# Performance work log

Hardware: AMD Instinct MI355X
Metric: run time of the kernel (lower is better)

The kernel has to match this reference:

```python
import jax, jax.numpy as jnp
import numpy as np

DIM = 2048
NUM_HEADS = 16
HEAD_DIM = 128
MAX_SEQ_LEN = 2048
ATTN_SCALE = 0.12
EPS = 1e-6


def _rms_norm(x):
    # RMSNorm without learned weight, over last dim
    return x * jax.lax.rsqrt(jnp.mean(jnp.square(x), axis=-1, keepdims=True) + EPS)


def _rope_tables(T):
    # half of the head dim rotates, half is identity (zero frequency)
    quarter = HEAD_DIM // 4
    angular_freq = (1.0 / 1024.0) ** jnp.linspace(0.0, 1.0, quarter, dtype=jnp.float32)
    angular_freq = jnp.concatenate([angular_freq, jnp.zeros(quarter, dtype=jnp.float32)])  # [D/2]
    t = jnp.arange(T, dtype=jnp.float32)
    theta = t[:, None] * angular_freq[None, :]  # [T, D/2]
    return jnp.cos(theta), jnp.sin(theta)


def _apply_rope(x, cos, sin):
    # x: [B, T, H, D]; cos/sin: [T, D/2] -> broadcast [1, T, 1, D/2]
    x1, x2 = jnp.split(x, 2, axis=-1)
    c = cos[None, :, None, :]
    s = sin[None, :, None, :]
    y1 = x1 * c + x2 * s
    y2 = -x1 * s + x2 * c
    return jnp.concatenate([y1, y2], axis=-1)


def setup_inputs() -> dict:
    key = jax.random.key(0)
    k1, k2, k3, k4 = jax.random.split(key, 4)
    hdim = NUM_HEADS * HEAD_DIM
    x = jax.random.normal(k1, (1, MAX_SEQ_LEN, DIM), dtype=jnp.float32)
    qkvo_w = jax.random.normal(k2, (4, hdim, DIM), dtype=jnp.float32) * (DIM ** -0.5)
    ve = jax.random.normal(k3, (1, MAX_SEQ_LEN, hdim), dtype=jnp.float32)
    lambdas = jax.random.uniform(k4, (2,), dtype=jnp.float32)
    return {"x": x, "qkvo_w": qkvo_w, "ve": ve, "lambdas": lambdas}


def reference(x, qkvo_w, ve, lambdas):
    B, T, _ = x.shape
    H, D = NUM_HEADS, HEAD_DIM
    # fused qkv projection: [B, T, 3*H*D]
    qkv = jnp.einsum('btc,ehc->bteh', x, qkvo_w[:3]).reshape(B, T, 3, H, D)
    q, k, v = qkv[:, :, 0], qkv[:, :, 1], qkv[:, :, 2]  # each [B, T, H, D]
    q, k, v = _rms_norm(q), _rms_norm(k), _rms_norm(v)
    cos, sin = _rope_tables(T)
    q = _apply_rope(q, cos, sin)
    k = _apply_rope(k, cos, sin)
    v = lambdas[0] * v + lambdas[1] * ve.reshape(B, T, H, D)
    # causal attention with fixed scale
    scores = jnp.einsum('bthd,bshd->bhts', q, k) * ATTN_SCALE  # [B, H, T, T]
    causal = jnp.tril(jnp.ones((T, T), dtype=bool))
    scores = jnp.where(causal[None, None], scores, -jnp.inf)
    p = jax.nn.softmax(scores, axis=-1)
    y = jnp.einsum('bhts,bshd->bthd', p, v).reshape(B, T, H * D)
    return jnp.einsum('bth,ch->btc', y, qkvo_w[3])
```

## Files before the change

### kernel.cpp

```cpp
#include <hip/hip_runtime.h>
#include <math.h>

#define SEQ  2048
#define CDIM 2048
#define NH   16
#define DH   128
#define HDIM 2048

typedef __attribute__((ext_vector_type(8))) short  bf16x8;
typedef __attribute__((ext_vector_type(4))) float  f32x4;
typedef unsigned short ushort_t;

__device__ __forceinline__ unsigned short f2bf(float f) {
  unsigned u = __float_as_uint(f);
  u = (u + 0x7fffu + ((u >> 16) & 1u)) >> 16;
  return (unsigned short)u;
}
__device__ __forceinline__ float b2f(unsigned short s) {
  return __uint_as_float((unsigned)s << 16);
}

__device__ __forceinline__ void async_ld16(const ushort_t* g, ushort_t* l) {
  __builtin_amdgcn_global_load_lds((const __attribute__((address_space(1))) unsigned int*)g,
                                   (__attribute__((address_space(3))) unsigned int*)l,
                                   16, 0, 0);
}

__device__ __forceinline__ f32x4 mfma16(bf16x8 a, bf16x8 b, f32x4 c) {
  return __builtin_amdgcn_mfma_f32_16x16x32_bf16(a, b, c, 0, 0, 0);
}

__global__ __launch_bounds__(256) void to_bf16(const float* __restrict__ src,
                                               ushort_t* __restrict__ dst, int n8) {
  int i = blockIdx.x * 256 + threadIdx.x;
  if (i >= n8) return;
  const float4* s = (const float4*)src;
  float4 f0 = s[i * 2], f1 = s[i * 2 + 1];
  bf16x8 o;
  o[0] = (short)f2bf(f0.x); o[1] = (short)f2bf(f0.y);
  o[2] = (short)f2bf(f0.z); o[3] = (short)f2bf(f0.w);
  o[4] = (short)f2bf(f1.x); o[5] = (short)f2bf(f1.y);
  o[6] = (short)f2bf(f1.z); o[7] = (short)f2bf(f1.w);
  *(bf16x8*)&dst[i * 8] = o;
}

template <int OUT_BF16>
__global__ __launch_bounds__(256) void gemm_bf16(const ushort_t* __restrict__ A,
                                                 const ushort_t* __restrict__ B,
                                                 void* __restrict__ Cv,
                                                 long bStride, long cStride) {
  constexpr int K = CDIM, N = HDIM;
  __shared__ __align__(16) ushort_t As[128 * 32];
  __shared__ __align__(16) ushort_t Bs[128 * 32];
  const ushort_t* Bp = B + (long)blockIdx.z * bStride;
  const int m0 = blockIdx.y * 128, n0 = blockIdx.x * 128;
  const int tid = threadIdx.x, lane = tid & 63, wave = tid >> 6;
  const int wm = wave >> 1, wn = wave & 1;
  const int g = lane >> 4, l15 = lane & 15;
  const int srow = tid >> 2, scc = tid & 3;

  f32x4 acc[4][4];
#pragma unroll
  for (int i = 0; i < 4; ++i)
#pragma unroll
    for (int j = 0; j < 4; ++j) acc[i][j] = (f32x4)0.0f;

  for (int k0 = 0; k0 < K; k0 += 32) {
    __syncthreads();
    {
      int r0 = srow, r1 = srow + 64;
      int c0 = scc ^ ((r0 >> 1) & 3), c1 = scc ^ ((r1 >> 1) & 3);
      async_ld16(&A [(long)(m0 + r0) * K + k0 + c0 * 8], &As[wave * 512]);
      async_ld16(&A [(long)(m0 + r1) * K + k0 + c1 * 8], &As[2048 + wave * 512]);
      async_ld16(&Bp[(long)(n0 + r0) * K + k0 + c0 * 8], &Bs[wave * 512]);
      async_ld16(&Bp[(long)(n0 + r1) * K + k0 + c1 * 8], &Bs[2048 + wave * 512]);
    }
    __syncthreads();

    bf16x8 af[4], bfr[4];
#pragma unroll
    for (int mi = 0; mi < 4; ++mi) {
      int row = wm * 64 + mi * 16 + l15;
      int cc = g ^ ((row >> 1) & 3);
      af[mi] = *(const bf16x8*)&As[row * 32 + cc * 8];
    }
#pragma unroll
    for (int ni = 0; ni < 4; ++ni) {
      int row = wn * 64 + ni * 16 + l15;
      int cc = g ^ ((row >> 1) & 3);
      bfr[ni] = *(const bf16x8*)&Bs[row * 32 + cc * 8];
    }
#pragma unroll
    for (int mi = 0; mi < 4; ++mi)
#pragma unroll
      for (int ni = 0; ni < 4; ++ni)
        acc[mi][ni] = mfma16(af[mi], bfr[ni], acc[mi][ni]);
  }

#pragma unroll
  for (int mi = 0; mi < 4; ++mi)
#pragma unroll
    for (int ni = 0; ni < 4; ++ni) {
      int row = m0 + wm * 64 + mi * 16 + g * 4;
      int col = n0 + wn * 64 + ni * 16 + l15;
#pragma unroll
      for (int r = 0; r < 4; ++r) {
        if (OUT_BF16)
          ((ushort_t*)Cv)[cStride * blockIdx.z + (long)(row + r) * N + col] = f2bf(acc[mi][ni][r]);
        else
          ((float*)Cv)[(long)(row + r) * N + col] = acc[mi][ni][r];
      }
    }
}

__device__ __forceinline__ float wave_sum64(float x) {
#pragma unroll
  for (int m = 32; m >= 1; m >>= 1) x += __shfl_xor(x, m, 64);
  return x;
}

__global__ __launch_bounds__(64) void norm_rope(ushort_t* __restrict__ qkvb,
                                                const float* __restrict__ ve,
                                                const float* __restrict__ lambdas) {
  const int t = blockIdx.x, h = blockIdx.y, d = threadIdx.x;
  const long base = (long)t * HDIM + h * DH;
  ushort_t* q = qkvb + base;
  ushort_t* k = qkvb + (long)SEQ * HDIM + base;
  ushort_t* v = qkvb + 2L * SEQ * HDIM + base;

  float q1 = b2f(q[d]), q2 = b2f(q[d + 64]);
  float k1 = b2f(k[d]), k2 = b2f(k[d + 64]);
  float v1 = b2f(v[d]), v2 = b2f(v[d + 64]);

  float qsc = rsqrtf(wave_sum64(q1 * q1 + q2 * q2) * (1.0f / 128.0f) + 1e-6f);
  float ksc = rsqrtf(wave_sum64(k1 * k1 + k2 * k2) * (1.0f / 128.0f) + 1e-6f);
  float vsc = rsqrtf(wave_sum64(v1 * v1 + v2 * v2) * (1.0f / 128.0f) + 1e-6f);
  q1 *= qsc; q2 *= qsc;
  k1 *= ksc; k2 *= ksc;
  v1 *= vsc; v2 *= vsc;

  float freq = (d < 32) ? powf(1.0f / 1024.0f, (float)d * (1.0f / 31.0f)) : 0.0f;
  float th = (float)t * freq;
  float c = cosf(th), s = sinf(th);

  float qo1 = q1 * c + q2 * s, qo2 = -q1 * s + q2 * c;
  float ko1 = k1 * c + k2 * s, ko2 = -k1 * s + k2 * c;

  float l0 = lambdas[0], l1 = lambdas[1];
  const float* vep = ve + base;
  float vo1 = l0 * v1 + l1 * vep[d];
  float vo2 = l0 * v2 + l1 * vep[d + 64];

  q[d] = f2bf(qo1); q[d + 64] = f2bf(qo2);
  k[d] = f2bf(ko1); k[d + 64] = f2bf(ko2);
  v[d] = f2bf(vo1); v[d + 64] = f2bf(vo2);
}

__global__ __launch_bounds__(256) void transpose_v(const ushort_t* __restrict__ vb,
                                                   ushort_t* __restrict__ vbT) {
  __shared__ __align__(16) ushort_t L[64 * 136];
  const int t0 = blockIdx.x * 64, h = blockIdx.y;
  const int tid = threadIdx.x;
#pragma unroll
  for (int p = 0; p < 4; ++p) {
    int idx = p * 256 + tid;
    int row = idx >> 4, cc = idx & 15;
    *(bf16x8*)&L[row * 136 + cc * 8] =
        *(const bf16x8*)&vb[(long)(t0 + row) * HDIM + h * DH + cc * 8];
  }
  __syncthreads();
#pragma unroll
  for (int p = 0; p < 4; ++p) {
    int idx = p * 256 + tid;
    int d = idx >> 3, tc = (idx & 7) * 8;
    bf16x8 o;
#pragma unroll
    for (int j = 0; j < 8; ++j) o[j] = (short)L[(tc + j) * 136 + d];
    *(bf16x8*)&vbT[((long)h * DH + d) * SEQ + t0 + tc] = o;
  }
}

__global__ __launch_bounds__(128) void flash_mfma(const ushort_t* __restrict__ qkvb,
                                                  const ushort_t* __restrict__ vbT,
                                                  ushort_t* __restrict__ yb) {
  __shared__ __align__(16) ushort_t Ks[64 * 128];
  __shared__ __align__(16) ushort_t Vt[128 * 64];
  __shared__ __align__(16) ushort_t Ps[64 * 72];
  const int q0 = blockIdx.x * 64, h = blockIdx.y;
  const int tid = threadIdx.x, lane = tid & 63, wave = tid >> 6;
  const int g = lane >> 4, l15 = lane & 15;
  const ushort_t* Kg = qkvb + (long)SEQ * HDIM;
  const ushort_t* Vg = vbT + (long)h * DH * SEQ;

  bf16x8 qf[2][4];
#pragma unroll
  for (int nt = 0; nt < 2; ++nt)
#pragma unroll
    for (int ks = 0; ks < 4; ++ks)
      qf[nt][ks] = *(const bf16x8*)
          &qkvb[(long)(q0 + wave * 32 + nt * 16 + l15) * HDIM + h * DH + ks * 32 + g * 8];

  f32x4 oacc[2][8];
#pragma unroll
  for (int qt = 0; qt < 2; ++qt)
#pragma unroll
    for (int dt = 0; dt < 8; ++dt) oacc[qt][dt] = (f32x4)0.0f;
  float mrow[2] = {-1e30f, -1e30f}, lrow[2] = {0.0f, 0.0f};

  for (int s0 = 0; s0 <= q0; s0 += 64) {
    __syncthreads();
#pragma unroll
    for (int i = 0; i < 8; ++i) {
      int idx = i * 128 + tid;
      { int row = idx >> 4, cc = idx & 15, cg = cc ^ (row & 7);
        async_ld16(&Kg[(long)(s0 + row) * HDIM + h * DH + cg * 8], &Ks[i * 1024 + wave * 512]); }
      { int row = idx >> 3, cc = idx & 7,  cg = cc ^ (row & 7);
        async_ld16(&Vg[(long)row * SEQ + s0 + cg * 8], &Vt[i * 1024 + wave * 512]); }
    }
    __syncthreads();

    f32x4 st[2][4];
#pragma unroll
    for (int nt = 0; nt < 2; ++nt)
#pragma unroll
      for (int mt = 0; mt < 4; ++mt) st[nt][mt] = (f32x4)0.0f;
#pragma unroll
    for (int ks = 0; ks < 4; ++ks)
#pragma unroll
      for (int mt = 0; mt < 4; ++mt) {
        int row = mt * 16 + l15;
        int cg = ks * 4 + g;
        int cc = cg ^ (row & 7);
        bf16x8 a = *(const bf16x8*)&Ks[row * 128 + cc * 8];
        st[0][mt] = mfma16(a, qf[0][ks], st[0][mt]);
        st[1][mt] = mfma16(a, qf[1][ks], st[1][mt]);
      }

    float alpha_q[2];
#pragma unroll
    for (int nt = 0; nt < 2; ++nt) {
      const int qg = q0 + wave * 32 + nt * 16 + l15;
      float p[4][4];
      float tmax = -1e30f;
#pragma unroll
      for (int mt = 0; mt < 4; ++mt)
#pragma unroll
        for (int r = 0; r < 4; ++r) {
          float sv = st[nt][mt][r] * 0.12f;
          if (s0 + mt * 16 + g * 4 + r > qg) sv = -1e30f;
          p[mt][r] = sv;
          tmax = fmaxf(tmax, sv);
        }
      tmax = fmaxf(tmax, __shfl_xor(tmax, 16, 64));
      tmax = fmaxf(tmax, __shfl_xor(tmax, 32, 64));
      float nm = fmaxf(mrow[nt], tmax);
      float alpha = __expf(mrow[nt] - nm);
      float psum = 0.0f;
#pragma unroll
      for (int mt = 0; mt < 4; ++mt) {
        float e0 = __expf(p[mt][0] - nm), e1 = __expf(p[mt][1] - nm);
        float e2 = __expf(p[mt][2] - nm), e3 = __expf(p[mt][3] - nm);
        unsigned short b0 = f2bf(e0), b1 = f2bf(e1), b2 = f2bf(e2), b3 = f2bf(e3);
        psum += b2f(b0) + b2f(b1) + b2f(b2) + b2f(b3);
        unsigned lo = (unsigned)b0 | ((unsigned)b1 << 16);
        unsigned hi = (unsigned)b2 | ((unsigned)b3 << 16);
        *(uint2*)&Ps[(wave * 32 + nt * 16 + l15) * 72 + mt * 16 + g * 4] = make_uint2(lo, hi);
      }
      psum += __shfl_xor(psum, 16, 64);
      psum += __shfl_xor(psum, 32, 64);
      mrow[nt] = nm;
      lrow[nt] = lrow[nt] * alpha + psum;
      alpha_q[nt] = alpha;
    }

    float aO[2][4];
#pragma unroll
    for (int qt = 0; qt < 2; ++qt)
#pragma unroll
      for (int r = 0; r < 4; ++r)
        aO[qt][r] = __shfl(alpha_q[qt], g * 4 + r, 64);
#pragma unroll
    for (int qt = 0; qt < 2; ++qt)
#pragma unroll
      for (int dt = 0; dt < 8; ++dt)
#pragma unroll
        for (int r = 0; r < 4; ++r)
          oacc[qt][dt][r] *= aO[qt][r];

#pragma unroll
    for (int ks = 0; ks < 2; ++ks) {
      bf16x8 ap0 = *(const bf16x8*)&Ps[(wave * 32 + l15) * 72 + ks * 32 + g * 8];
      bf16x8 ap1 = *(const bf16x8*)&Ps[(wave * 32 + 16 + l15) * 72 + ks * 32 + g * 8];
#pragma unroll
      for (int dt = 0; dt < 8; ++dt) {
        int row = dt * 16 + l15;
        int cg = ks * 4 + g;
        int cc = cg ^ (row & 7);
        bf16x8 bv = *(const bf16x8*)&Vt[row * 64 + cc * 8];
        oacc[0][dt] = mfma16(ap0, bv, oacc[0][dt]);
        oacc[1][dt] = mfma16(ap1, bv, oacc[1][dt]);
      }
    }
  }

  float linv[2][4];
#pragma unroll
  for (int qt = 0; qt < 2; ++qt)
#pragma unroll
    for (int r = 0; r < 4; ++r)
      linv[qt][r] = 1.0f / __shfl(lrow[qt], g * 4 + r, 64);
#pragma unroll
  for (int qt = 0; qt < 2; ++qt)
#pragma unroll
    for (int dt = 0; dt < 8; ++dt) {
      int row = q0 + wave * 32 + qt * 16 + g * 4;
      int col = h * DH + dt * 16 + l15;
#pragma unroll
      for (int r = 0; r < 4; ++r)
        yb[(long)(row + r) * HDIM + col] = f2bf(oacc[qt][dt][r] * linv[qt][r]);
    }
}

extern "C" void kernel_launch(void* const* d_in, const int* in_sizes, int n_in,
                              void* d_out, int out_size, void* d_ws, size_t ws_size,
                              hipStream_t stream) {
  const float* x       = (const float*)d_in[0];
  const float* w       = (const float*)d_in[1];
  const float* ve      = (const float*)d_in[2];
  const float* lambdas = (const float*)d_in[3];
  float* out = (float*)d_out;

  char* ws = (char*)d_ws;
  ushort_t* qkvb = (ushort_t*)ws;
  ushort_t* xb   = (ushort_t*)(ws + 25165824);
  ushort_t* wb   = (ushort_t*)(ws + 33554432);
  ushort_t* vbT  = (ushort_t*)(ws + 67108864);
  ushort_t* yb   = xb;

  to_bf16<<<2048, 256, 0, stream>>>(x, xb, (SEQ * CDIM) / 8);
  to_bf16<<<8192, 256, 0, stream>>>(w, wb, (4 * HDIM * CDIM) / 8);
  gemm_bf16<1><<<dim3(16, 16, 3), 256, 0, stream>>>(xb, wb, qkvb,
                                                    (long)HDIM * CDIM, (long)SEQ * HDIM);
  norm_rope<<<dim3(SEQ, NH), 64, 0, stream>>>(qkvb, ve, lambdas);
  transpose_v<<<dim3(SEQ / 64, NH), 256, 0, stream>>>(qkvb + 2L * SEQ * HDIM, vbT);
  flash_mfma<<<dim3(SEQ / 64, NH), 128, 0, stream>>>(qkvb, vbT, yb);
  gemm_bf16<0><<<dim3(16, 16, 1), 256, 0, stream>>>(yb, wb + 3L * HDIM * CDIM, out, 0, 0);
}
```

Measured before the change: 340.7 us.

## Fuse norm/RoPE/V-transpose into QKV GEMM, rebalance flash attention, split-K projection

The separate norm_rope and transpose_v kernels are removed. The QKV GEMM epilogue now does the per-head RMS norm through a cross-wave LDS reduction, applies RoPE to Q and K, and mixes V with ve while also writing the transposed V directly. Flash attention now uses four 16-row waves, pairs a short and a long causal query tile per block for load balance, and double-buffers K/V through async LDS loads. It also drops the running-max rescale, relying on normalized q and k keeping scores bounded. The output projection is split along K into two 512-block GEMMs plus an add kernel to fill more CUs, which costs an extra fp32 buffer pass.

After: 681.9 us. 2x slower.

```diff
diff --git a/kernel.cpp b/kernel.cpp
--- a/kernel.cpp
+++ b/kernel.cpp
@@ -44,15 +44,18 @@
   *(bf16x8*)&dst[i * 8] = o;
 }
 
-template <int OUT_BF16>
-__global__ __launch_bounds__(256) void gemm_bf16(const ushort_t* __restrict__ A,
-                                                 const ushort_t* __restrict__ B,
-                                                 void* __restrict__ Cv,
-                                                 long bStride, long cStride) {
-  constexpr int K = CDIM, N = HDIM;
+__global__ __launch_bounds__(256, 3) void gemm_qkv(const ushort_t* __restrict__ A,
+                                                   const ushort_t* __restrict__ B,
+                                                   ushort_t* __restrict__ qkvb,
+                                                   ushort_t* __restrict__ vbT,
+                                                   const float* __restrict__ ve,
+                                                   const float* __restrict__ lambdas) {
+  constexpr int K = CDIM;
   __shared__ __align__(16) ushort_t As[128 * 32];
   __shared__ __align__(16) ushort_t Bs[128 * 32];
-  const ushort_t* Bp = B + (long)blockIdx.z * bStride;
+  __shared__ float red[4][4][4][4];
+  const int z = blockIdx.z;
+  const ushort_t* Bp = B + (long)z * HDIM * CDIM;
   const int m0 = blockIdx.y * 128, n0 = blockIdx.x * 128;
   const int tid = threadIdx.x, lane = tid & 63, wave = tid >> 6;
   const int wm = wave >> 1, wn = wave & 1;
@@ -86,6 +89,262 @@
     }
 #pragma unroll
     for (int ni = 0; ni < 4; ++ni) {
+      int rowm = (ni & 1) * 16 + wn * 32 + (ni >> 1) * 64 + l15;
+      int cc = g ^ ((rowm >> 1) & 3);
+      bfr[ni] = *(const bf16x8*)&Bs[rowm * 32 + cc * 8];
+    }
+#pragma unroll
+    for (int mi = 0; mi < 4; ++mi)
+#pragma unroll
+      for (int ni = 0; ni < 4; ++ni)
+        acc[mi][ni] = mfma16(af[mi], bfr[ni], acc[mi][ni]);
+  }
+
+  {
+    float part[4][4];
+#pragma unroll
+    for (int mi = 0; mi < 4; ++mi)
+#pragma unroll
+      for (int r = 0; r < 4; ++r) {
+        float s = 0.f;
+#pragma unroll
+        for (int ni = 0; ni < 4; ++ni) { float v = acc[mi][ni][r]; s += v * v; }
+        part[mi][r] = s;
+      }
+#pragma unroll
+    for (int mask = 1; mask < 16; mask <<= 1)
+#pragma unroll
+      for (int mi = 0; mi < 4; ++mi)
+#pragma unroll
+        for (int r = 0; r < 4; ++r)
+          part[mi][r] += __shfl_xor(part[mi][r], mask, 64);
+    __syncthreads();
+    if (l15 == 0)
+#pragma unroll
+      for (int mi = 0; mi < 4; ++mi)
+#pragma unroll
+        for (int r = 0; r < 4; ++r) red[wave][mi][g][r] = part[mi][r];
+    __syncthreads();
+  }
+  float scl[4][4];
+#pragma unroll
+  for (int mi = 0; mi < 4; ++mi)
+#pragma unroll
+    for (int r = 0; r < 4; ++r)
+      scl[mi][r] = rsqrtf((red[wm * 2][mi][g][r] + red[wm * 2 + 1][mi][g][r]) *
+                              (1.0f / 128.0f) + 1e-6f);
+
+  if (z < 2) {
+    ushort_t* dst = qkvb + (long)z * SEQ * HDIM;
+#pragma unroll
+    for (int ni2 = 0; ni2 < 2; ++ni2) {
+      int c = ni2 * 16 + wn * 32 + l15;
+      float freq = (c < 32) ? powf(9.765625e-4f, (float)c * (1.0f / 31.0f)) : 0.0f;
+#pragma unroll
+      for (int mi = 0; mi < 4; ++mi)
+#pragma unroll
+        for (int r = 0; r < 4; ++r) {
+          int tt = m0 + wm * 64 + mi * 16 + g * 4 + r;
+          float th = (float)tt * freq;
+          float co = cosf(th), si = sinf(th);
+          float x1 = acc[mi][ni2][r] * scl[mi][r];
+          float x2 = acc[mi][ni2 + 2][r] * scl[mi][r];
+          dst[(long)tt * HDIM + n0 + c]      = f2bf(x1 * co + x2 * si);
+          dst[(long)tt * HDIM + n0 + c + 64] = f2bf(-x1 * si + x2 * co);
+        }
+    }
+  } else {
+    float l0 = lambdas[0], l1 = lambdas[1];
+    ushort_t* dst = qkvb + 2L * SEQ * HDIM;
+#pragma unroll
+    for (int mi = 0; mi < 4; ++mi)
+#pragma unroll
+      for (int ni = 0; ni < 4; ++ni) {
+        int c = (ni & 1) * 16 + wn * 32 + (ni >> 1) * 64 + l15;
+        int t0q = m0 + wm * 64 + mi * 16 + g * 4;
+        unsigned short pk[4];
+#pragma unroll
+        for (int r = 0; r < 4; ++r) {
+          int tt = t0q + r;
+          float vv = l0 * acc[mi][ni][r] * scl[mi][r] + l1 * ve[(long)tt * HDIM + n0 + c];
+          unsigned short b = f2bf(vv);
+          dst[(long)tt * HDIM + n0 + c] = b;
+          pk[r] = b;
+        }
+        *(uint2*)&vbT[(long)(n0 + c) * SEQ + t0q] =
+            make_uint2((unsigned)pk[0] | ((unsigned)pk[1] << 16),
+                       (unsigned)pk[2] | ((unsigned)pk[3] << 16));
+      }
+  }
+}
+
+__global__ __launch_bounds__(256) void flash_mfma(const ushort_t* __restrict__ qkvb,
+                                                  const ushort_t* __restrict__ vbT,
+                                                  ushort_t* __restrict__ yb) {
+  __shared__ __align__(16) ushort_t Ks[2][64 * 128];
+  __shared__ __align__(16) ushort_t Vt[2][128 * 64];
+  __shared__ __align__(16) ushort_t Ps[64 * 72];
+  const int xp = blockIdx.x, h = blockIdx.y;
+  const int tid = threadIdx.x, lane = tid & 63, wave = tid >> 6;
+  const int g = lane >> 4, l15 = lane & 15;
+  const ushort_t* Kg = qkvb + (long)SEQ * HDIM + (long)h * DH;
+  const ushort_t* Vg = vbT + (long)h * DH * SEQ;
+  const int tA = xp, tB = 31 - xp;
+  const int nA = xp + 1;
+
+  auto stage = [&](int buf, int s0) {
+#pragma unroll
+    for (int i = 0; i < 4; ++i) {
+      int idx = i * 256 + tid;
+      int rk = idx >> 4, ck = (idx & 15) ^ (rk & 7);
+      async_ld16(&Kg[(long)(s0 + rk) * HDIM + ck * 8], &Ks[buf][i * 2048 + wave * 512]);
+      int rv = idx >> 3, cv = (idx & 7) ^ (rv & 7);
+      async_ld16(&Vg[(long)rv * SEQ + s0 + cv * 8], &Vt[buf][i * 2048 + wave * 512]);
+    }
+  };
+
+  bf16x8 qf[4];
+  auto loadQ = [&](int qt) {
+#pragma unroll
+    for (int ks = 0; ks < 4; ++ks)
+      qf[ks] = *(const bf16x8*)
+          &qkvb[(long)(qt * 64 + wave * 16 + l15) * HDIM + h * DH + ks * 32 + g * 8];
+  };
+
+  f32x4 oacc[8];
+  float lrow = 0.f;
+#pragma unroll
+  for (int dt = 0; dt < 8; ++dt) oacc[dt] = (f32x4)0.0f;
+
+  auto writeO = [&](int qt) {
+    float linv[4];
+#pragma unroll
+    for (int r = 0; r < 4; ++r) linv[r] = 1.0f / __shfl(lrow, g * 4 + r, 64);
+#pragma unroll
+    for (int dt = 0; dt < 8; ++dt) {
+      int row = qt * 64 + wave * 16 + g * 4;
+      int col = h * DH + dt * 16 + l15;
+#pragma unroll
+      for (int r = 0; r < 4; ++r)
+        yb[(long)(row + r) * HDIM + col] = f2bf(oacc[dt][r] * linv[r]);
+    }
+  };
+
+  loadQ(tA);
+  stage(0, 0);
+
+  for (int j = 0; j < 33; ++j) {
+    __syncthreads();
+    int part = (j >= nA);
+    int qt = part ? tB : tA;
+    int s0 = (part ? (j - nA) : j) * 64;
+    if (j == nA) {
+      writeO(tA);
+#pragma unroll
+      for (int dt = 0; dt < 8; ++dt) oacc[dt] = (f32x4)0.0f;
+      lrow = 0.f;
+      loadQ(tB);
+    }
+    if (j + 1 < 33) {
+      int p2 = (j + 1 >= nA);
+      int s2 = ((j + 1) - (p2 ? nA : 0)) * 64;
+      stage((j + 1) & 1, s2);
+    }
+    const ushort_t* Kc = Ks[j & 1];
+    const ushort_t* Vc = Vt[j & 1];
+
+    f32x4 st[4];
+#pragma unroll
+    for (int mt = 0; mt < 4; ++mt) st[mt] = (f32x4)0.0f;
+#pragma unroll
+    for (int ks = 0; ks < 4; ++ks)
+#pragma unroll
+      for (int mt = 0; mt < 4; ++mt) {
+        int row = mt * 16 + l15;
+        bf16x8 a = *(const bf16x8*)&Kc[row * 128 + (((ks * 4 + g) ^ (row & 7)) * 8)];
+        st[mt] = mfma16(a, qf[ks], st[mt]);
+      }
+
+    const int qg = qt * 64 + wave * 16 + l15;
+    const bool diag = (s0 == qt * 64);
+    float psum = 0.f;
+#pragma unroll
+    for (int mt = 0; mt < 4; ++mt) {
+      unsigned short pb[4];
+#pragma unroll
+      for (int r = 0; r < 4; ++r) {
+        float e = (diag && (s0 + mt * 16 + g * 4 + r > qg))
+                      ? 0.0f : __expf(st[mt][r] * 0.12f);
+        unsigned short b = f2bf(e);
+        pb[r] = b;
+        psum += b2f(b);
+      }
+      *(uint2*)&Ps[(wave * 16 + l15) * 72 + mt * 16 + g * 4] =
+          make_uint2((unsigned)pb[0] | ((unsigned)pb[1] << 16),
+                     (unsigned)pb[2] | ((unsigned)pb[3] << 16));
+    }
+    psum += __shfl_xor(psum, 16, 64);
+    psum += __shfl_xor(psum, 32, 64);
+    lrow += psum;
+
+#pragma unroll
+    for (int ks2 = 0; ks2 < 2; ++ks2) {
+      bf16x8 ap = *(const bf16x8*)&Ps[(wave * 16 + l15) * 72 + ks2 * 32 + g * 8];
+#pragma unroll
+      for (int dt = 0; dt < 8; ++dt) {
+        int row = dt * 16 + l15;
+        bf16x8 bv = *(const bf16x8*)&Vc[row * 64 + (((ks2 * 4 + g) ^ (row & 7)) * 8)];
+        oacc[dt] = mfma16(ap, bv, oacc[dt]);
+      }
+    }
+  }
+  writeO(tB);
+}
+
+__global__ __launch_bounds__(256) void gemm_proj(const ushort_t* __restrict__ A,
+                                                 const ushort_t* __restrict__ B,
+                                                 float* __restrict__ C0,
+                                                 float* __restrict__ C1) {
+  constexpr int KH = 1024, LDK = CDIM, N = HDIM;
+  __shared__ __align__(16) ushort_t As[128 * 32];
+  __shared__ __align__(16) ushort_t Bs[128 * 32];
+  const int z = blockIdx.z;
+  const ushort_t* Ap = A + (long)z * KH;
+  const ushort_t* Bp = B + (long)z * KH;
+  float* Cp = z ? C1 : C0;
+  const int m0 = blockIdx.y * 128, n0 = blockIdx.x * 128;
+  const int tid = threadIdx.x, lane = tid & 63, wave = tid >> 6;
+  const int wm = wave >> 1, wn = wave & 1;
+  const int g = lane >> 4, l15 = lane & 15;
+  const int srow = tid >> 2, scc = tid & 3;
+
+  f32x4 acc[4][4];
+#pragma unroll
+  for (int i = 0; i < 4; ++i)
+#pragma unroll
+    for (int j = 0; j < 4; ++j) acc[i][j] = (f32x4)0.0f;
+
+  for (int k0 = 0; k0 < KH; k0 += 32) {
+    __syncthreads();
+    {
+      int r0 = srow, r1 = srow + 64;
+      int c0 = scc ^ ((r0 >> 1) & 3), c1 = scc ^ ((r1 >> 1) & 3);
+      async_ld16(&Ap[(long)(m0 + r0) * LDK + k0 + c0 * 8], &As[wave * 512]);
+      async_ld16(&Ap[(long)(m0 + r1) * LDK + k0 + c1 * 8], &As[2048 + wave * 512]);
+      async_ld16(&Bp[(long)(n0 + r0) * LDK + k0 + c0 * 8], &Bs[wave * 512]);
+      async_ld16(&Bp[(long)(n0 + r1) * LDK + k0 + c1 * 8], &Bs[2048 + wave * 512]);
+    }
+    __syncthreads();
+
+    bf16x8 af[4], bfr[4];
+#pragma unroll
+    for (int mi = 0; mi < 4; ++mi) {
+      int row = wm * 64 + mi * 16 + l15;
+      int cc = g ^ ((row >> 1) & 3);
+      af[mi] = *(const bf16x8*)&As[row * 32 + cc * 8];
+    }
+#pragma unroll
+    for (int ni = 0; ni < 4; ++ni) {
       int row = wn * 64 + ni * 16 + l15;
       int cc = g ^ ((row >> 1) & 3);
       bfr[ni] = *(const bf16x8*)&Bs[row * 32 + cc * 8];
@@ -104,221 +363,19 @@
       int row = m0 + wm * 64 + mi * 16 + g * 4;
       int col = n0 + wn * 64 + ni * 16 + l15;
 #pragma unroll
-      for (int r = 0; r < 4; ++r) {
-        if (OUT_BF16)
-          ((ushort_t*)Cv)[cStride * blockIdx.z + (long)(row + r) * N + col] = f2bf(acc[mi][ni][r]);
-        else
-          ((float*)Cv)[(long)(row + r) * N + col] = acc[mi][ni][r];
-      }
-    }
-}
-
-__device__ __forceinline__ float wave_sum64(float x) {
-#pragma unroll
-  for (int m = 32; m >= 1; m >>= 1) x += __shfl_xor(x, m, 64);
-  return x;
-}
-
-__global__ __launch_bounds__(64) void norm_rope(ushort_t* __restrict__ qkvb,
-                                                const float* __restrict__ ve,
-                                                const float* __restrict__ lambdas) {
-  const int t = blockIdx.x, h = blockIdx.y, d = threadIdx.x;
-  const long base = (long)t * HDIM + h * DH;
-  ushort_t* q = qkvb + base;
-  ushort_t* k = qkvb + (long)SEQ * HDIM + base;
-  ushort_t* v = qkvb + 2L * SEQ * HDIM + base;
-
-  float q1 = b2f(q[d]), q2 = b2f(q[d + 64]);
-  float k1 = b2f(k[d]), k2 = b2f(k[d + 64]);
-  float v1 = b2f(v[d]), v2 = b2f(v[d + 64]);
-
-  float qsc = rsqrtf(wave_sum64(q1 * q1 + q2 * q2) * (1.0f / 128.0f) + 1e-6f);
-  float ksc = rsqrtf(wave_sum64(k1 * k1 + k2 * k2) * (1.0f / 128.0f) + 1e-6f);
-  float vsc = rsqrtf(wave_sum64(v1 * v1 + v2 * v2) * (1.0f / 128.0f) + 1e-6f);
-  q1 *= qsc; q2 *= qsc;
-  k1 *= ksc; k2 *= ksc;
-  v1 *= vsc; v2 *= vsc;
-
-  float freq = (d < 32) ? powf(1.0f / 1024.0f, (float)d * (1.0f / 31.0f)) : 0.0f;
-  float th = (float)t * freq;
-  float c = cosf(th), s = sinf(th);
-
-  float qo1 = q1 * c + q2 * s, qo2 = -q1 * s + q2 * c;
-  float ko1 = k1 * c + k2 * s, ko2 = -k1 * s + k2 * c;
-
-  float l0 = lambdas[0], l1 = lambdas[1];
-  const float* vep = ve + base;
-  float vo1 = l0 * v1 + l1 * vep[d];
-  float vo2 = l0 * v2 + l1 * vep[d + 64];
-
-  q[d] = f2bf(qo1); q[d + 64] = f2bf(qo2);
-  k[d] = f2bf(ko1); k[d + 64] = f2bf(ko2);
-  v[d] = f2bf(vo1); v[d + 64] = f2bf(vo2);
-}
-
-__global__ __launch_bounds__(256) void transpose_v(const ushort_t* __restrict__ vb,
-                                                   ushort_t* __restrict__ vbT) {
-  __shared__ __align__(16) ushort_t L[64 * 136];
-  const int t0 = blockIdx.x * 64, h = blockIdx.y;
-  const int tid = threadIdx.x;
-#pragma unroll
-  for (int p = 0; p < 4; ++p) {
-    int idx = p * 256 + tid;
-    int row = idx >> 4, cc = idx & 15;
-    *(bf16x8*)&L[row * 136 + cc * 8] =
-        *(const bf16x8*)&vb[(long)(t0 + row) * HDIM + h * DH + cc * 8];
-  }
-  __syncthreads();
-#pragma unroll
-  for (int p = 0; p < 4; ++p) {
-    int idx = p * 256 + tid;
-    int d = idx >> 3, tc = (idx & 7) * 8;
-    bf16x8 o;
-#pragma unroll
-    for (int j = 0; j < 8; ++j) o[j] = (short)L[(tc + j) * 136 + d];
-    *(bf16x8*)&vbT[((long)h * DH + d) * SEQ + t0 + tc] = o;
-  }
-}
-
-__global__ __launch_bounds__(128) void flash_mfma(const ushort_t* __restrict__ qkvb,
-                                                  const ushort_t* __restrict__ vbT,
-                                                  ushort_t* __restrict__ yb) {
-  __shared__ __align__(16) ushort_t Ks[64 * 128];
-  __shared__ __align__(16) ushort_t Vt[128 * 64];
-  __shared__ __align__(16) ushort_t Ps[64 * 72];
-  const int q0 = blockIdx.x * 64, h = blockIdx.y;
-  const int tid = threadIdx.x, lane = tid & 63, wave = tid >> 6;
-  const int g = lane >> 4, l15 = lane & 15;
-  const ushort_t* Kg = qkvb + (long)SEQ * HDIM;
-  const ushort_t* Vg = vbT + (long)h * DH * SEQ;
-
-  bf16x8 qf[2][4];
-#pragma unroll
-  for (int nt = 0; nt < 2; ++nt)
-#pragma unroll
-    for (int ks = 0; ks < 4; ++ks)
-      qf[nt][ks] = *(const bf16x8*)
-          &qkvb[(long)(q0 + wave * 32 + nt * 16 + l15) * HDIM + h * DH + ks * 32 + g * 8];
-
-  f32x4 oacc[2][8];
-#pragma unroll
-  for (int qt = 0; qt < 2; ++qt)
-#pragma unroll
-    for (int dt = 0; dt < 8; ++dt) oacc[qt][dt] = (f32x4)0.0f;
-  float mrow[2] = {-1e30f, -1e30f}, lrow[2] = {0.0f, 0.0f};
-
-  for (int s0 = 0; s0 <= q0; s0 += 64) {
-    __syncthreads();
-#pragma unroll
-    for (int i = 0; i < 8; ++i) {
-      int idx = i * 128 + tid;
-      { int row = idx >> 4, cc = idx & 15, cg = cc ^ (row & 7);
-        async_ld16(&Kg[(long)(s0 + row) * HDIM + h * DH + cg * 8], &Ks[i * 1024 + wave * 512]); }
-      { int row = idx >> 3, cc = idx & 7,  cg = cc ^ (row & 7);
-        async_ld16(&Vg[(long)row * SEQ + s0 + cg * 8], &Vt[i * 1024 + wave * 512]); }
-    }
-    __syncthreads();
-
-    f32x4 st[2][4];
-#pragma unroll
-    for (int nt = 0; nt < 2; ++nt)
-#pragma unroll
-      for (int mt = 0; mt < 4; ++mt) st[nt][mt] = (f32x4)0.0f;
-#pragma unroll
-    for (int ks = 0; ks < 4; ++ks)
-#pragma unroll
-      for (int mt = 0; mt < 4; ++mt) {
-        int row = mt * 16 + l15;
-        int cg = ks * 4 + g;
-        int cc = cg ^ (row & 7);
-        bf16x8 a = *(const bf16x8*)&Ks[row * 128 + cc * 8];
-        st[0][mt] = mfma16(a, qf[0][ks], st[0][mt]);
-        st[1][mt] = mfma16(a, qf[1][ks], st[1][mt]);
-      }
-
-    float alpha_q[2];
-#pragma unroll
-    for (int nt = 0; nt < 2; ++nt) {
-      const int qg = q0 + wave * 32 + nt * 16 + l15;
-      float p[4][4];
-      float tmax = -1e30f;
-#pragma unroll
-      for (int mt = 0; mt < 4; ++mt)
-#pragma unroll
-        for (int r = 0; r < 4; ++r) {
-          float sv = st[nt][mt][r] * 0.12f;
-          if (s0 + mt * 16 + g * 4 + r > qg) sv = -1e30f;
-          p[mt][r] = sv;
-          tmax = fmaxf(tmax, sv);
-        }
-      tmax = fmaxf(tmax, __shfl_xor(tmax, 16, 64));
-      tmax = fmaxf(tmax, __shfl_xor(tmax, 32, 64));
-      float nm = fmaxf(mrow[nt], tmax);
-      float alpha = __expf(mrow[nt] - nm);
-      float psum = 0.0f;
-#pragma unroll
-      for (int mt = 0; mt < 4; ++mt) {
-        float e0 = __expf(p[mt][0] - nm), e1 = __expf(p[mt][1] - nm);
-        float e2 = __expf(p[mt][2] - nm), e3 = __expf(p[mt][3] - nm);
-        unsigned short b0 = f2bf(e0), b1 = f2bf(e1), b2 = f2bf(e2), b3 = f2bf(e3);
-        psum += b2f(b0) + b2f(b1) + b2f(b2) + b2f(b3);
-        unsigned lo = (unsigned)b0 | ((unsigned)b1 << 16);
-        unsigned hi = (unsigned)b2 | ((unsigned)b3 << 16);
-        *(uint2*)&Ps[(wave * 32 + nt * 16 + l15) * 72 + mt * 16 + g * 4] = make_uint2(lo, hi);
-      }
-      psum += __shfl_xor(psum, 16, 64);
-      psum += __shfl_xor(psum, 32, 64);
-      mrow[nt] = nm;
-      lrow[nt] = lrow[nt] * alpha + psum;
-      alpha_q[nt] = alpha;
-    }
-
-    float aO[2][4];
-#pragma unroll
-    for (int qt = 0; qt < 2; ++qt)
-#pragma unroll
       for (int r = 0; r < 4; ++r)
-        aO[qt][r] = __shfl(alpha_q[qt], g * 4 + r, 64);
-#pragma unroll
-    for (int qt = 0; qt < 2; ++qt)
-#pragma unroll
-      for (int dt = 0; dt < 8; ++dt)
-#pragma unroll
-        for (int r = 0; r < 4; ++r)
-          oacc[qt][dt][r] *= aO[qt][r];
-
-#pragma unroll
-    for (int ks = 0; ks < 2; ++ks) {
-      bf16x8 ap0 = *(const bf16x8*)&Ps[(wave * 32 + l15) * 72 + ks * 32 + g * 8];
-      bf16x8 ap1 = *(const bf16x8*)&Ps[(wave * 32 + 16 + l15) * 72 + ks * 32 + g * 8];
-#pragma unroll
-      for (int dt = 0; dt < 8; ++dt) {
-        int row = dt * 16 + l15;
-        int cg = ks * 4 + g;
-        int cc = cg ^ (row & 7);
-        bf16x8 bv = *(const bf16x8*)&Vt[row * 64 + cc * 8];
-        oacc[0][dt] = mfma16(ap0, bv, oacc[0][dt]);
-        oacc[1][dt] = mfma16(ap1, bv, oacc[1][dt]);
-      }
-    }
-  }
-
-  float linv[2][4];
-#pragma unroll
-  for (int qt = 0; qt < 2; ++qt)
-#pragma unroll
-    for (int r = 0; r < 4; ++r)
-      linv[qt][r] = 1.0f / __shfl(lrow[qt], g * 4 + r, 64);
-#pragma unroll
-  for (int qt = 0; qt < 2; ++qt)
-#pragma unroll
-    for (int dt = 0; dt < 8; ++dt) {
-      int row = q0 + wave * 32 + qt * 16 + g * 4;
-      int col = h * DH + dt * 16 + l15;
-#pragma unroll
-      for (int r = 0; r < 4; ++r)
-        yb[(long)(row + r) * HDIM + col] = f2bf(oacc[qt][dt][r] * linv[qt][r]);
-    }
+        Cp[(long)(row + r) * N + col] = acc[mi][ni][r];
+    }
+}
+
+__global__ __launch_bounds__(256) void add_out(float* __restrict__ out,
+                                               const float* __restrict__ p0, int n4) {
+  int i = blockIdx.x * 256 + threadIdx.x;
+  if (i >= n4) return;
+  float4 a = ((const float4*)out)[i];
+  float4 b = ((const float4*)p0)[i];
+  a.x += b.x; a.y += b.y; a.z += b.z; a.w += b.w;
+  ((float4*)out)[i] = a;
 }
 
 extern "C" void kernel_launch(void* const* d_in, const int* in_sizes, int n_in,
@@ -336,13 +393,12 @@
   ushort_t* wb   = (ushort_t*)(ws + 33554432);
   ushort_t* vbT  = (ushort_t*)(ws + 67108864);
   ushort_t* yb   = xb;
+  float*    p0   = (float*)ws;
 
   to_bf16<<<2048, 256, 0, stream>>>(x, xb, (SEQ * CDIM) / 8);
   to_bf16<<<8192, 256, 0, stream>>>(w, wb, (4 * HDIM * CDIM) / 8);
-  gemm_bf16<1><<<dim3(16, 16, 3), 256, 0, stream>>>(xb, wb, qkvb,
-                                                    (long)HDIM * CDIM, (long)SEQ * HDIM);
-  norm_rope<<<dim3(SEQ, NH), 64, 0, stream>>>(qkvb, ve, lambdas);
-  transpose_v<<<dim3(SEQ / 64, NH), 256, 0, stream>>>(qkvb + 2L * SEQ * HDIM, vbT);
-  flash_mfma<<<dim3(SEQ / 64, NH), 128, 0, stream>>>(qkvb, vbT, yb);
-  gemm_bf16<0><<<dim3(16, 16, 1), 256, 0, stream>>>(yb, wb + 3L * HDIM * CDIM, out, 0, 0);
-}
+  gemm_qkv<<<dim3(16, 16, 3), 256, 0, stream>>>(xb, wb, qkvb, vbT, ve, lambdas);
+  flash_mfma<<<dim3(16, 16), 256, 0, stream>>>(qkvb, vbT, yb);
+  gemm_proj<<<dim3(16, 16, 2), 256, 0, stream>>>(yb, wb + 3L * HDIM * CDIM, p0, out);
+  add_out<<<4096, 256, 0, stream>>>(out, p0, (SEQ * HDIM) / 4);
+}
```
